# Kernel optimization log

Measured on AMD Instinct MI355X. Metric: run time of the kernel, lower is better.

## Reference

```python
import jax, jax.numpy as jnp
import numpy as np

N, E, D, H, L = 4096, 131072, 2048, 4, 2  # nodes, edges, embed_dim, heads, layers
HD = D // H


def setup_inputs() -> dict:
    key = jax.random.key(0)
    ks = jax.random.split(key, 11)
    s = 0.02
    feats = jax.random.normal(ks[0], (N, D), jnp.float32)
    edge_index = jax.random.randint(ks[1], (E, 2), 0, N, dtype=jnp.int32)
    # per-layer linear params, stored as [in, out] so y = x @ W + b (== torch x @ W.T + b)
    Wq = jax.random.normal(ks[2], (L, D, D), jnp.float32) * s
    Wk = jax.random.normal(ks[3], (L, D, D), jnp.float32) * s
    Wv = jax.random.normal(ks[4], (L, D, D), jnp.float32) * s
    Wo = jax.random.normal(ks[5], (L, D, D), jnp.float32) * s
    bq = jnp.zeros((L, D), jnp.float32)
    bk = jnp.zeros((L, D), jnp.float32)
    bv = jnp.zeros((L, D), jnp.float32)
    bo = jnp.zeros((L, D), jnp.float32)
    return dict(feats=feats, Wq=Wq, bq=bq, Wk=Wk, bk=bk, Wv=Wv, bv=bv,
                Wo=Wo, bo=bo, edge_index=edge_index)


def _gnn_forward(feats, Wq, bq, Wk, bk, Wv, bv, Wo, bo, row, col):
    n = feats.shape[0]
    # dense edge mask [1, N, N] (masked_fill where mask == 0 -> -10000)
    mask = jnp.zeros((n, n), bool).at[row, col].set(True)[None]
    scale = 1.0 / jnp.sqrt(jnp.asarray(HD, feats.dtype))
    x = feats
    for l in range(L):
        q = (x @ Wq[l] + bq[l]).reshape(n, H, HD).transpose(1, 0, 2)  # [H,N,d]
        k = (x @ Wk[l] + bk[l]).reshape(n, H, HD).transpose(1, 0, 2)
        v = (x @ Wv[l] + bv[l]).reshape(n, H, HD).transpose(1, 0, 2)
        scores = jnp.einsum('hnd,hmd->hnm', q, k) * scale          # [H,N,N]
        scores = jnp.where(mask, scores, jnp.asarray(-10000.0, scores.dtype))
        attn = jax.nn.softmax(scores, axis=-1)                      # [H,N,N]
        se = attn[:, row, col]                                      # [H,E] gather per-edge
        out_e = se[:, :, None] * v[:, col]                          # [H,E,d]
        agg = jax.vmap(lambda o: jax.ops.segment_sum(o, row, num_segments=n))(out_e)  # [H,N,d]
        x = agg.transpose(1, 0, 2).reshape(n, H * HD) @ Wo[l] + bo[l]
    return x


def reference(feats, Wq, bq, Wk, bk, Wv, bv, Wo, bo, edge_index):
    row, col = edge_index[:, 0], edge_index[:, 1]
    return _gnn_forward(feats, Wq, bq, Wk, bk, Wv, bv, Wo, bo, row, col)
```

## Files before the change

### kernel.cpp

```cpp
#include <hip/hip_runtime.h>
#include <hip/hip_bf16.h>

typedef unsigned short u16;
typedef unsigned int u32;
typedef short bf16x8 __attribute__((ext_vector_type(8)));
typedef float f32x4 __attribute__((ext_vector_type(4)));
typedef unsigned short u16x4 __attribute__((ext_vector_type(4)));
typedef unsigned short u16x8 __attribute__((ext_vector_type(8)));
typedef float f32x4v __attribute__((ext_vector_type(4)));

#define NN 4096
#define DD 2048
#define HH 4
#define HDIM 512
#define EE 131072
#define NB 512
#define EBS 256

__device__ __forceinline__ float bf2f(u16 x) {
    return __uint_as_float(((u32)x) << 16);
}
__device__ __forceinline__ u16 f2bf(float f) {
    u32 u = __float_as_uint(f);
    u += 0x7fffu + ((u >> 16) & 1u);
    return (u16)(u >> 16);
}

#define GLOAD16(g, l)                                                          \
    __builtin_amdgcn_global_load_lds(                                          \
        (const __attribute__((address_space(1))) void*)(g),                    \
        (__attribute__((address_space(3))) void*)(l), 16, 0, 0)

__global__ __launch_bounds__(256) void k_cvt(const float* __restrict__ in,
                                             u16* __restrict__ out, int n4)
{
    int i = blockIdx.x * 256 + threadIdx.x;
    if (i >= n4) return;
    f32x4v v = *(const f32x4v*)&in[i * 4];
    u16x4 o;
#pragma unroll
    for (int j = 0; j < 4; j++) o[j] = f2bf(v[j]);
    *(u16x4*)&out[i * 4] = o;
}

template <bool OUTF32>
__global__ __launch_bounds__(512, 2) void k_gemm256(
    const u16* __restrict__ A, const u16* __restrict__ Bt,
    const float* __restrict__ bias, void* __restrict__ Cout,
    int M, int Ncols, int K)
{
    extern __shared__ u16 lds[];
    u16* sA = lds;
    u16* sB = lds + 3 * 16384;

    int t = threadIdx.x;
    int wid = t >> 6, lane = t & 63;
    int wr = wid >> 1, wc = wid & 1;
    int l15 = lane & 15, kg = lane >> 4;

    int flat = blockIdx.y * gridDim.x + blockIdx.x;
    int per = (gridDim.x * gridDim.y) >> 3;
    int nid = (flat & 7) * per + (flat >> 3);
    int bm = nid / gridDim.x;
    int bn = nid % gridDim.x;

    const int NT = K >> 6;

    int trow = t >> 3;
    int scolE = ((t & 7) ^ (trow & 7)) * 8;
    const u16* Abase = A + ((size_t)(bm * 256) + trow) * K + scolE;
    const u16* Bbase = Bt + ((size_t)(bn * 128) + trow) * K + scolE;

#define STAGE_A(buf, TT, j)                                                    \
    GLOAD16(Abase + (size_t)(j) * 64 * K + (size_t)(TT) * 64,                  \
            sA + (buf) * 16384 + (j) * 4096 + t * 8)
#define STAGE_B(buf, TT, j)                                                    \
    GLOAD16(Bbase + (size_t)(j) * 64 * K + (size_t)(TT) * 64,                  \
            sB + (buf) * 8192 + (j) * 4096 + t * 8)

    int s8_0 = ((0 * 4 + kg) ^ (l15 & 7)) * 8;
    int s8_1 = ((1 * 4 + kg) ^ (l15 & 7)) * 8;

    f32x4 acc[4][4];
#pragma unroll
    for (int m = 0; m < 4; m++)
#pragma unroll
        for (int n = 0; n < 4; n++) acc[m][n] = (f32x4){0.f, 0.f, 0.f, 0.f};

#pragma unroll
    for (int j = 0; j < 4; j++) STAGE_A(0, 0, j);
#pragma unroll
    for (int j = 0; j < 2; j++) STAGE_B(0, 0, j);
#pragma unroll
    for (int j = 0; j < 4; j++) STAGE_A(1, 1, j);
#pragma unroll
    for (int j = 0; j < 2; j++) STAGE_B(1, 1, j);
    asm volatile("s_waitcnt vmcnt(6)" ::: "memory");
    __builtin_amdgcn_s_barrier();

    int bufc = 0;
    for (int T = 0; T < NT; ++T) {
        const u16* bA = sA + bufc * 16384;
        const u16* bB = sB + bufc * 8192;
        int nxt2 = bufc + 2; if (nxt2 >= 3) nxt2 -= 3;
        bool st = (T + 2 < NT);
#pragma unroll
        for (int q = 0; q < 4; ++q) {
            const int qm = q >> 1, qn = q & 1;
            bf16x8 afr[2][2], bfr[2][2];
#pragma unroll
            for (int i = 0; i < 2; ++i) {
                int ra = wr * 64 + (qm * 2 + i) * 16 + l15;
                afr[i][0] = *(const bf16x8*)(bA + ra * 64 + s8_0);
                afr[i][1] = *(const bf16x8*)(bA + ra * 64 + s8_1);
                int rb = wc * 64 + (qn * 2 + i) * 16 + l15;
                bfr[i][0] = *(const bf16x8*)(bB + rb * 64 + s8_0);
                bfr[i][1] = *(const bf16x8*)(bB + rb * 64 + s8_1);
            }
            if (st) {
                if (q == 0)      { STAGE_A(nxt2, T + 2, 0); STAGE_A(nxt2, T + 2, 1); }
                else if (q == 1) { STAGE_A(nxt2, T + 2, 2); STAGE_A(nxt2, T + 2, 3); }
                else if (q == 2) { STAGE_B(nxt2, T + 2, 0); STAGE_B(nxt2, T + 2, 1); }
            }
            __builtin_amdgcn_s_barrier();
            __builtin_amdgcn_s_setprio(1);
#pragma unroll
            for (int i = 0; i < 2; ++i)
#pragma unroll
                for (int j = 0; j < 2; ++j) {
                    acc[qm * 2 + i][qn * 2 + j] = __builtin_amdgcn_mfma_f32_16x16x32_bf16(
                        afr[i][0], bfr[j][0], acc[qm * 2 + i][qn * 2 + j], 0, 0, 0);
                    acc[qm * 2 + i][qn * 2 + j] = __builtin_amdgcn_mfma_f32_16x16x32_bf16(
                        afr[i][1], bfr[j][1], acc[qm * 2 + i][qn * 2 + j], 0, 0, 0);
                }
            __builtin_amdgcn_s_setprio(0);
            if (q == 3) {
                if (T + 2 < NT)
                    asm volatile("s_waitcnt vmcnt(6)" ::: "memory");
                else if (T + 1 < NT)
                    asm volatile("s_waitcnt vmcnt(0)" ::: "memory");
            }
            if (!(T == NT - 1 && q == 3)) __builtin_amdgcn_s_barrier();
        }
        bufc += 1; if (bufc >= 3) bufc -= 3;
    }
#undef STAGE_A
#undef STAGE_B

    int row0 = bm * 256 + wr * 64 + kg * 4;
    int col0 = bn * 128 + wc * 64 + l15;
#pragma unroll
    for (int n = 0; n < 4; n++) {
        int cc = col0 + n * 16;
        float bv = bias[cc];
#pragma unroll
        for (int m = 0; m < 4; m++) {
            int rb = row0 + m * 16;
#pragma unroll
            for (int r = 0; r < 4; r++) {
                float v = acc[m][n][r] + bv;
                if (OUTF32)
                    ((float*)Cout)[(size_t)(rb + r) * Ncols + cc] = v;
                else
                    ((u16*)Cout)[(size_t)(rb + r) * Ncols + cc] = f2bf(v);
            }
        }
    }
}

__global__ void k_wtrans(const float* __restrict__ Wq, const float* __restrict__ Wk,
                         const float* __restrict__ Wv, const float* __restrict__ Wo,
                         int loff, u16* __restrict__ Wt)
{
    int z = blockIdx.z;
    const float* W = (z == 0) ? Wq : (z == 1) ? Wk : (z == 2) ? Wv : Wo;
    u16* out = Wt + (size_t)z * DD * DD;
    __shared__ u16 tile[32][33];
    int tx = threadIdx.x, ty = threadIdx.y;
    int x = blockIdx.x * 32 + tx;
    int y0 = blockIdx.y * 32;
#pragma unroll
    for (int j = 0; j < 32; j += 8)
        tile[ty + j][tx] = f2bf(W[loff + (size_t)(y0 + ty + j) * DD + x]);
    __syncthreads();
    int ox = blockIdx.y * 32 + tx;
    int oy0 = blockIdx.x * 32;
#pragma unroll
    for (int j = 0; j < 32; j += 8)
        out[(size_t)(oy0 + ty + j) * DD + ox] = tile[tx][ty + j];
}

__global__ __launch_bounds__(256) void k_hist(const int* __restrict__ ei,
                                              int* __restrict__ blockcnt)
{
    __shared__ int h[NN];
    int b = blockIdx.x, t = threadIdx.x;
    for (int i = t; i < NN; i += 256) h[i] = 0;
    __syncthreads();
    int2 e = ((const int2*)ei)[b * EBS + t];
    atomicAdd(&h[e.x], 1);
    __syncthreads();
    for (int i = t; i < NN; i += 256) blockcnt[(size_t)b * NN + i] = h[i];
}

__global__ void k_rowscan(int* __restrict__ blockcnt, int* __restrict__ rowsum)
{
    int i = blockIdx.x * 256 + threadIdx.x;
    int run = 0;
    for (int b = 0; b < NB; b++) {
        int v = blockcnt[(size_t)b * NN + i];
        blockcnt[(size_t)b * NN + i] = run;
        run += v;
    }
    rowsum[i] = run;
}

__global__ __launch_bounds__(1024) void k_scan2(const int* __restrict__ rowsum,
                                                int* __restrict__ rstart)
{
    __shared__ int sh[1024];
    int t = threadIdx.x;
    int v[4], pre[4], s = 0;
#pragma unroll
    for (int j = 0; j < 4; j++) v[j] = rowsum[t * 4 + j];
#pragma unroll
    for (int j = 0; j < 4; j++) { pre[j] = s; s += v[j]; }
    sh[t] = s;
    __syncthreads();
    for (int off = 1; off < 1024; off <<= 1) {
        int x = (t >= off) ? sh[t - off] : 0;
        __syncthreads();
        sh[t] += x;
        __syncthreads();
    }
    int bp = (t == 0) ? 0 : sh[t - 1];
#pragma unroll
    for (int j = 0; j < 4; j++) rstart[t * 4 + j] = bp + pre[j];
    if (t == 1023) rstart[NN] = sh[1023];
}

__global__ __launch_bounds__(256) void k_scatter2(
    const int* __restrict__ ei, const int* __restrict__ blockcnt,
    const int* __restrict__ rstart, int* __restrict__ srow,
    int* __restrict__ scol)
{
    __shared__ int rsh[EBS];
    int b = blockIdx.x, t = threadIdx.x;
    int2 e = ((const int2*)ei)[b * EBS + t];
    rsh[t] = e.x;
    __syncthreads();
    int rank = 0;
    for (int j = 0; j < t; j++) rank += (rsh[j] == e.x);
    int pos = rstart[e.x] + blockcnt[(size_t)b * NN + e.x] + rank;
    srow[pos] = e.x;
    scol[pos] = e.y;
}

__global__ __launch_bounds__(64) void k_flags(const int* __restrict__ scol,
                                              const int* __restrict__ rstart,
                                              int* __restrict__ flags)
{
    int i = blockIdx.x;
    int start = rstart[i], end = rstart[i + 1];
    int d = end - start;
    __shared__ int sc[1024];
    int lane = threadIdx.x;
    for (int j = lane; j < d && j < 1024; j += 64) sc[j] = scol[start + j];
    __syncthreads();
    for (int j = lane; j < d; j += 64) {
        int cj = (j < 1024) ? sc[j] : scol[start + j];
        int f = 1;
        for (int q = 0; q < j; ++q) {
            int cq = (q < 1024) ? sc[q] : scol[start + q];
            if (cq == cj) { f = 0; break; }
        }
        flags[start + j] = f;
    }
}

__global__ __launch_bounds__(256) void k_scores(
    const u16* __restrict__ Qb, const u16* __restrict__ Kb,
    const int* __restrict__ srow, const int* __restrict__ scol,
    float* __restrict__ pexp)
{
    int p = blockIdx.x * 4 + (threadIdx.x >> 6);
    int lane = threadIdx.x & 63;
    int r = srow[p], c = scol[p];
    const float scale = 0.04419417382415922f;
#pragma unroll
    for (int h = 0; h < HH; ++h) {
        u16x8 q8 = *(const u16x8*)&Qb[(size_t)r * DD + h * HDIM + lane * 8];
        u16x8 k8 = *(const u16x8*)&Kb[(size_t)c * DD + h * HDIM + lane * 8];
        float s = 0.f;
#pragma unroll
        for (int j = 0; j < 8; j++) s += bf2f(q8[j]) * bf2f(k8[j]);
#pragma unroll
        for (int off = 32; off > 0; off >>= 1) s += __shfl_xor(s, off, 64);
        if (lane == 0) pexp[p * 4 + h] = expf(s * scale);
    }
}

__global__ __launch_bounds__(256) void k_agg(
    const float* __restrict__ pexp, const int* __restrict__ flags,
    const int* __restrict__ scol, const int* __restrict__ rstart,
    const u16* __restrict__ Vb, u16* __restrict__ Aggb)
{
    int i = blockIdx.x;
    int start = rstart[i], end = rstart[i + 1];
    int h = threadIdx.x >> 6, lane = threadIdx.x & 63;
    __shared__ float sden[HH];
    float dsum = 0.f;
    for (int p = start + lane; p < end; p += 64)
        if (flags[p]) dsum += pexp[p * 4 + h];
#pragma unroll
    for (int off = 32; off > 0; off >>= 1) dsum += __shfl_xor(dsum, off, 64);
    if (lane == 0) sden[h] = dsum;
    __syncthreads();
    float inv = (end > start) ? 1.0f / sden[h] : 0.0f;
    float acc[8] = {0.f, 0.f, 0.f, 0.f, 0.f, 0.f, 0.f, 0.f};
    for (int p = start; p < end; ++p) {
        float wgt = pexp[p * 4 + h] * inv;
        int c = scol[p];
        u16x8 v8 = *(const u16x8*)&Vb[(size_t)c * DD + h * HDIM + lane * 8];
#pragma unroll
        for (int j = 0; j < 8; j++) acc[j] += wgt * bf2f(v8[j]);
    }
    u16x8 o;
#pragma unroll
    for (int j = 0; j < 8; j++) o[j] = f2bf(acc[j]);
    *(u16x8*)&Aggb[(size_t)i * DD + h * HDIM + lane * 8] = o;
}

extern "C" void kernel_launch(void* const* d_in, const int* in_sizes, int n_in,
                              void* d_out, int out_size, void* d_ws, size_t ws_size,
                              hipStream_t stream)
{
    const float* feats = (const float*)d_in[0];
    const float* Wq = (const float*)d_in[1];
    const float* bq = (const float*)d_in[2];
    const float* Wk = (const float*)d_in[3];
    const float* bk = (const float*)d_in[4];
    const float* Wv = (const float*)d_in[5];
    const float* bv = (const float*)d_in[6];
    const float* Wo = (const float*)d_in[7];
    const float* bo = (const float*)d_in[8];
    const int* ei = (const int*)d_in[9];
    float* out = (float*)d_out;

    size_t off = 0;
    auto alloc = [&](size_t bytes) {
        void* p = (char*)d_ws + off;
        off += (bytes + 255) & ~(size_t)255;
        return p;
    };
    const size_t ND = (size_t)NN * DD;
    u16* Xb = (u16*)alloc(ND * 2);
    u16* Qb = (u16*)alloc(ND * 2);
    u16* Kb = (u16*)alloc(ND * 2);
    u16* Vb = (u16*)alloc(ND * 2);
    u16* Ab = (u16*)alloc(ND * 2);
    u16* Wt = (u16*)alloc((size_t)4 * DD * DD * 2);
    float* pexp = (float*)alloc((size_t)EE * HH * 4);
    int* blockcnt = (int*)alloc((size_t)NB * NN * 4);
    int* rowsum = (int*)alloc((size_t)NN * 4);
    int* rstart = (int*)alloc((size_t)(NN + 1) * 4);
    int* srow = (int*)alloc((size_t)EE * 4);
    int* scol = (int*)alloc((size_t)EE * 4);
    int* flags = (int*)alloc((size_t)EE * 4);
    (void)ws_size; (void)in_sizes; (void)n_in; (void)out_size;

    const int GEMM_LDS = 3 * (16384 + 8192) * 2;
    hipFuncSetAttribute((const void*)k_gemm256<false>,
                        hipFuncAttributeMaxDynamicSharedMemorySize, GEMM_LDS);
    hipFuncSetAttribute((const void*)k_gemm256<true>,
                        hipFuncAttributeMaxDynamicSharedMemorySize, GEMM_LDS);

    k_hist<<<NB, 256, 0, stream>>>(ei, blockcnt);
    k_rowscan<<<NN / 256, 256, 0, stream>>>(blockcnt, rowsum);
    k_scan2<<<1, 1024, 0, stream>>>(rowsum, rstart);
    k_scatter2<<<NB, 256, 0, stream>>>(ei, blockcnt, rstart, srow, scol);
    k_flags<<<NN, 64, 0, stream>>>(scol, rstart, flags);

    k_cvt<<<(int)(ND / 4 / 256), 256, 0, stream>>>(feats, Xb, (int)(ND / 4));

    dim3 gg(DD / 128, NN / 256);
    for (int l = 0; l < 2; ++l) {
        k_wtrans<<<dim3(DD / 32, DD / 32, 4), dim3(32, 8), 0, stream>>>(
            Wq, Wk, Wv, Wo, l * DD * DD, Wt);
        k_gemm256<false><<<gg, 512, GEMM_LDS, stream>>>(Xb, Wt + 0 * (size_t)DD * DD, bq + l * DD, Qb, NN, DD, DD);
        k_gemm256<false><<<gg, 512, GEMM_LDS, stream>>>(Xb, Wt + 1 * (size_t)DD * DD, bk + l * DD, Kb, NN, DD, DD);
        k_gemm256<false><<<gg, 512, GEMM_LDS, stream>>>(Xb, Wt + 2 * (size_t)DD * DD, bv + l * DD, Vb, NN, DD, DD);
        k_scores<<<EE / 4, 256, 0, stream>>>(Qb, Kb, srow, scol, pexp);
        k_agg<<<NN, 256, 0, stream>>>(pexp, flags, scol, rstart, Vb, Ab);
        if (l == 1) {
            k_gemm256<true><<<gg, 512, GEMM_LDS, stream>>>(Ab, Wt + 3 * (size_t)DD * DD, bo + l * DD, out, NN, DD, DD);
        } else {
            k_gemm256<false><<<gg, 512, GEMM_LDS, stream>>>(Ab, Wt + 3 * (size_t)DD * DD, bo + l * DD, Xb, NN, DD, DD);
        }
    }
}
```

Baseline: 731.2 us.

## Fuse Q/K/V projections into one GEMM and restructure score and MFMA loops

Replaces the three separate Q, K and V GEMM launches with a single GEMM over the concatenated transposed weights, writing an interleaved QKV buffer with row stride 6144 and picking the bias per column range. This cuts launch count and tail effects and gives one larger grid. The GEMM inner loop now loads B fragments once per half-tile instead of per quarter, and the barrier count per K-step drops from four to two, at the cost of more live registers. The scores kernel computes all four heads in one wave (16 lanes per head) with shorter shuffle reductions.

After: 696.7 us. 4.7% less time.

```diff
diff --git a/kernel.cpp b/kernel.cpp
--- a/kernel.cpp
+++ b/kernel.cpp
@@ -16,6 +16,7 @@
 #define EE 131072
 #define NB 512
 #define EBS 256
+#define QS 6144
 
 __device__ __forceinline__ float bf2f(u16 x) {
     return __uint_as_float(((u32)x) << 16);
@@ -46,7 +47,8 @@
 template <bool OUTF32>
 __global__ __launch_bounds__(512, 2) void k_gemm256(
     const u16* __restrict__ A, const u16* __restrict__ Bt,
-    const float* __restrict__ bias, void* __restrict__ Cout,
+    const float* __restrict__ bias0, const float* __restrict__ bias1,
+    const float* __restrict__ bias2, void* __restrict__ Cout,
     int M, int Ncols, int K)
 {
     extern __shared__ u16 lds[];
@@ -105,42 +107,47 @@
         int nxt2 = bufc + 2; if (nxt2 >= 3) nxt2 -= 3;
         bool st = (T + 2 < NT);
 #pragma unroll
-        for (int q = 0; q < 4; ++q) {
-            const int qm = q >> 1, qn = q & 1;
-            bf16x8 afr[2][2], bfr[2][2];
+        for (int qm = 0; qm < 2; ++qm) {
+            bf16x8 afr[2][2], bfr[2][2][2];
 #pragma unroll
             for (int i = 0; i < 2; ++i) {
                 int ra = wr * 64 + (qm * 2 + i) * 16 + l15;
                 afr[i][0] = *(const bf16x8*)(bA + ra * 64 + s8_0);
                 afr[i][1] = *(const bf16x8*)(bA + ra * 64 + s8_1);
-                int rb = wc * 64 + (qn * 2 + i) * 16 + l15;
-                bfr[i][0] = *(const bf16x8*)(bB + rb * 64 + s8_0);
-                bfr[i][1] = *(const bf16x8*)(bB + rb * 64 + s8_1);
             }
+#pragma unroll
+            for (int qn = 0; qn < 2; ++qn)
+#pragma unroll
+                for (int i = 0; i < 2; ++i) {
+                    int rb = wc * 64 + (qn * 2 + i) * 16 + l15;
+                    bfr[qn][i][0] = *(const bf16x8*)(bB + rb * 64 + s8_0);
+                    bfr[qn][i][1] = *(const bf16x8*)(bB + rb * 64 + s8_1);
+                }
             if (st) {
-                if (q == 0)      { STAGE_A(nxt2, T + 2, 0); STAGE_A(nxt2, T + 2, 1); }
-                else if (q == 1) { STAGE_A(nxt2, T + 2, 2); STAGE_A(nxt2, T + 2, 3); }
-                else if (q == 2) { STAGE_B(nxt2, T + 2, 0); STAGE_B(nxt2, T + 2, 1); }
+                if (qm == 0) { STAGE_A(nxt2, T + 2, 0); STAGE_A(nxt2, T + 2, 1); STAGE_A(nxt2, T + 2, 2); }
+                else         { STAGE_A(nxt2, T + 2, 3); STAGE_B(nxt2, T + 2, 0); STAGE_B(nxt2, T + 2, 1); }
             }
             __builtin_amdgcn_s_barrier();
             __builtin_amdgcn_s_setprio(1);
 #pragma unroll
-            for (int i = 0; i < 2; ++i)
-#pragma unroll
-                for (int j = 0; j < 2; ++j) {
-                    acc[qm * 2 + i][qn * 2 + j] = __builtin_amdgcn_mfma_f32_16x16x32_bf16(
-                        afr[i][0], bfr[j][0], acc[qm * 2 + i][qn * 2 + j], 0, 0, 0);
-                    acc[qm * 2 + i][qn * 2 + j] = __builtin_amdgcn_mfma_f32_16x16x32_bf16(
-                        afr[i][1], bfr[j][1], acc[qm * 2 + i][qn * 2 + j], 0, 0, 0);
-                }
+            for (int qn = 0; qn < 2; ++qn)
+#pragma unroll
+                for (int i = 0; i < 2; ++i)
+#pragma unroll
+                    for (int j = 0; j < 2; ++j) {
+                        acc[qm * 2 + i][qn * 2 + j] = __builtin_amdgcn_mfma_f32_16x16x32_bf16(
+                            afr[i][0], bfr[qn][j][0], acc[qm * 2 + i][qn * 2 + j], 0, 0, 0);
+                        acc[qm * 2 + i][qn * 2 + j] = __builtin_amdgcn_mfma_f32_16x16x32_bf16(
+                            afr[i][1], bfr[qn][j][1], acc[qm * 2 + i][qn * 2 + j], 0, 0, 0);
+                    }
             __builtin_amdgcn_s_setprio(0);
-            if (q == 3) {
+            if (qm == 1) {
                 if (T + 2 < NT)
                     asm volatile("s_waitcnt vmcnt(6)" ::: "memory");
                 else if (T + 1 < NT)
                     asm volatile("s_waitcnt vmcnt(0)" ::: "memory");
             }
-            if (!(T == NT - 1 && q == 3)) __builtin_amdgcn_s_barrier();
+            if (!(T == NT - 1 && qm == 1)) __builtin_amdgcn_s_barrier();
         }
         bufc += 1; if (bufc >= 3) bufc -= 3;
     }
@@ -152,7 +159,9 @@
 #pragma unroll
     for (int n = 0; n < 4; n++) {
         int cc = col0 + n * 16;
-        float bv = bias[cc];
+        int sel = cc >> 11;
+        const float* bp = (sel == 0) ? bias0 : (sel == 1) ? bias1 : bias2;
+        float bv = bp[cc & 2047];
 #pragma unroll
         for (int m = 0; m < 4; m++) {
             int rb = row0 + m * 16;
@@ -285,19 +294,26 @@
 {
     int p = blockIdx.x * 4 + (threadIdx.x >> 6);
     int lane = threadIdx.x & 63;
+    int h = lane >> 4, l16 = lane & 15;
     int r = srow[p], c = scol[p];
     const float scale = 0.04419417382415922f;
-#pragma unroll
-    for (int h = 0; h < HH; ++h) {
-        u16x8 q8 = *(const u16x8*)&Qb[(size_t)r * DD + h * HDIM + lane * 8];
-        u16x8 k8 = *(const u16x8*)&Kb[(size_t)c * DD + h * HDIM + lane * 8];
-        float s = 0.f;
-#pragma unroll
-        for (int j = 0; j < 8; j++) s += bf2f(q8[j]) * bf2f(k8[j]);
-#pragma unroll
-        for (int off = 32; off > 0; off >>= 1) s += __shfl_xor(s, off, 64);
-        if (lane == 0) pexp[p * 4 + h] = expf(s * scale);
-    }
+    const u16* qrow = Qb + (size_t)r * QS + h * HDIM + l16 * 8;
+    const u16* krow = Kb + (size_t)c * QS + h * HDIM + l16 * 8;
+    float sx = 0.f, sy = 0.f;
+#pragma unroll
+    for (int ch = 0; ch < 4; ++ch) {
+        u16x8 q8 = *(const u16x8*)(qrow + ch * 128);
+        u16x8 k8 = *(const u16x8*)(krow + ch * 128);
+#pragma unroll
+        for (int j = 0; j < 8; j += 2) {
+            sx += bf2f(q8[j]) * bf2f(k8[j]);
+            sy += bf2f(q8[j + 1]) * bf2f(k8[j + 1]);
+        }
+    }
+    float s = sx + sy;
+#pragma unroll
+    for (int off = 1; off < 16; off <<= 1) s += __shfl_xor(s, off, 64);
+    if (l16 == 0) pexp[p * 4 + h] = expf(s * scale);
 }
 
 __global__ __launch_bounds__(256) void k_agg(
@@ -321,7 +337,7 @@
     for (int p = start; p < end; ++p) {
         float wgt = pexp[p * 4 + h] * inv;
         int c = scol[p];
-        u16x8 v8 = *(const u16x8*)&Vb[(size_t)c * DD + h * HDIM + lane * 8];
+        u16x8 v8 = *(const u16x8*)&Vb[(size_t)c * QS + h * HDIM + lane * 8];
 #pragma unroll
         for (int j = 0; j < 8; j++) acc[j] += wgt * bf2f(v8[j]);
     }
@@ -355,9 +371,7 @@
     };
     const size_t ND = (size_t)NN * DD;
     u16* Xb = (u16*)alloc(ND * 2);
-    u16* Qb = (u16*)alloc(ND * 2);
-    u16* Kb = (u16*)alloc(ND * 2);
-    u16* Vb = (u16*)alloc(ND * 2);
+    u16* QKV = (u16*)alloc((size_t)NN * QS * 2);
     u16* Ab = (u16*)alloc(ND * 2);
     u16* Wt = (u16*)alloc((size_t)4 * DD * DD * 2);
     float* pexp = (float*)alloc((size_t)EE * HH * 4);
@@ -383,19 +397,21 @@
 
     k_cvt<<<(int)(ND / 4 / 256), 256, 0, stream>>>(feats, Xb, (int)(ND / 4));
 
-    dim3 gg(DD / 128, NN / 256);
+    dim3 gqkv(QS / 128, NN / 256);
+    dim3 go(DD / 128, NN / 256);
     for (int l = 0; l < 2; ++l) {
         k_wtrans<<<dim3(DD / 32, DD / 32, 4), dim3(32, 8), 0, stream>>>(
             Wq, Wk, Wv, Wo, l * DD * DD, Wt);
-        k_gemm256<false><<<gg, 512, GEMM_LDS, stream>>>(Xb, Wt + 0 * (size_t)DD * DD, bq + l * DD, Qb, NN, DD, DD);
-        k_gemm256<false><<<gg, 512, GEMM_LDS, stream>>>(Xb, Wt + 1 * (size_t)DD * DD, bk + l * DD, Kb, NN, DD, DD);
-        k_gemm256<false><<<gg, 512, GEMM_LDS, stream>>>(Xb, Wt + 2 * (size_t)DD * DD, bv + l * DD, Vb, NN, DD, DD);
-        k_scores<<<EE / 4, 256, 0, stream>>>(Qb, Kb, srow, scol, pexp);
-        k_agg<<<NN, 256, 0, stream>>>(pexp, flags, scol, rstart, Vb, Ab);
+        k_gemm256<false><<<gqkv, 512, GEMM_LDS, stream>>>(
+            Xb, Wt, bq + l * DD, bk + l * DD, bv + l * DD, QKV, NN, QS, DD);
+        k_scores<<<EE / 4, 256, 0, stream>>>(QKV, QKV + DD, srow, scol, pexp);
+        k_agg<<<NN, 256, 0, stream>>>(pexp, flags, scol, rstart, QKV + 2 * DD, Ab);
         if (l == 1) {
-            k_gemm256<true><<<gg, 512, GEMM_LDS, stream>>>(Ab, Wt + 3 * (size_t)DD * DD, bo + l * DD, out, NN, DD, DD);
+            k_gemm256<true><<<go, 512, GEMM_LDS, stream>>>(
+                Ab, Wt + 3 * (size_t)DD * DD, bo + l * DD, bo + l * DD, bo + l * DD, out, NN, DD, DD);
         } else {
-            k_gemm256<false><<<gg, 512, GEMM_LDS, stream>>>(Ab, Wt + 3 * (size_t)DD * DD, bo + l * DD, Xb, NN, DD, DD);
+            k_gemm256<false><<<go, 512, GEMM_LDS, stream>>>(
+                Ab, Wt + 3 * (size_t)DD * DD, bo + l * DD, bo + l * DD, bo + l * DD, Xb, NN, DD, DD);
         }
     }
 }
```
